# Kernel optimization log

Measured on AMD Instinct MI355X. Metric: run time of the kernel, lower is better.

The kernel has to match this reference:

```python
import jax, jax.numpy as jnp
import numpy as np

SR = 48000
SEG = 960
NH = 8
BASE = 440.0
F0_MIN = 20.0
F0_MAX = 16000.0
EPS = 1e-4
N, C, LF = 16, 256, 200


def _interp_linear(x, Lw):
    # Matches torch F.interpolate(mode='linear', align_corners=False).
    # x: (N, C, Lf) -> (N, C, Lw)
    Lf = x.shape[-1]
    scale = Lf / Lw
    src = (jnp.arange(Lw, dtype=x.dtype) + 0.5) * scale - 0.5
    src = jnp.clip(src, 0.0, Lf - 1)
    i0 = jnp.floor(src).astype(jnp.int32)
    i1 = jnp.minimum(i0 + 1, Lf - 1)
    w = src - i0.astype(x.dtype)
    return x[..., i0] * (1.0 - w) + x[..., i1] * w


def setup_inputs() -> dict:
    key = jax.random.key(0)
    ks = jax.random.split(key, 7)
    scale = 1.0 / np.sqrt(C)
    return {
        "x": jax.random.normal(ks[0], (N, C, LF), dtype=jnp.float32),
        "mag_w": jax.random.uniform(ks[1], (NH, C), jnp.float32, -scale, scale),
        "mag_b": jax.random.uniform(ks[2], (NH,), jnp.float32, -scale, scale),
        "cn_scale": jnp.ones((1, C, 1), jnp.float32),
        "cn_shift": jnp.zeros((1, C, 1), jnp.float32),
        "oct_w": jax.random.uniform(ks[3], (1, C), jnp.float32, -scale, scale),
        "oct_b": jax.random.uniform(ks[4], (1,), jnp.float32, -scale, scale),
    }


def reference(x, mag_w, mag_b, cn_scale, cn_shift, oct_w, oct_b):
    n, c, Lf = x.shape
    Lw = Lf * SEG
    # ChannelNorm (torch.std is unbiased -> ddof=1)
    mu = jnp.mean(x, axis=1, keepdims=True)
    sigma = jnp.std(x, axis=1, keepdims=True, ddof=1) + EPS
    xn = (x - mu) / sigma * cn_scale + cn_shift
    # 1x1 convs
    octave = jnp.einsum('ncl,oc->nol', xn, oct_w) + oct_b[None, :, None]  # (N,1,Lf)
    mag = jnp.exp(jnp.minimum(jnp.einsum('ncl,hc->nhl', x, mag_w) + mag_b[None, :, None], 6.0))  # (N,NH,Lf)
    f0 = jnp.clip(BASE * jnp.exp2(octave), F0_MIN, F0_MAX)  # (N,1,Lf)
    mul = jnp.arange(1, NH + 1, dtype=x.dtype)[None, :, None]
    formants = f0 * mul  # (N,NH,Lf)
    formants_w = _interp_linear(formants, Lw)  # (N,NH,Lw)
    mag_w_up = _interp_linear(mag, Lw)         # (N,NH,Lw)
    t = jnp.cumsum(formants_w / SR, axis=2)
    harmonics = jnp.sin(2.0 * jnp.pi * t) * mag_w_up
    wave = jnp.mean(harmonics, axis=1, keepdims=True)  # (N,1,Lw)
    return wave
```

## Files before the change

kernel.cpp:

```cpp
#include <hip/hip_runtime.h>
#include <math.h>


#define NB   16
#define CCH  256
#define LFR  200
#define LW   192000
#define NHH  8
#define NKM  201
#define INV_SR (1.0 / 48000.0)
#define PSTRIDE 20

__device__ inline double wave_sum64(double v) {
    #pragma unroll
    for (int off = 32; off > 0; off >>= 1) v += __shfl_xor(v, off);
    return v;
}
__device__ inline double wave_incl_scan64(double v) {
    int lane = threadIdx.x & 63;
    #pragma unroll
    for (int off = 1; off < 64; off <<= 1) {
        double t = __shfl_up(v, off);
        if (lane >= off) v += t;
    }
    return v;
}

__global__ __launch_bounds__(1024)
void hg_prep(const float* __restrict__ x,
             const float* __restrict__ mag_w, const float* __restrict__ mag_b,
             const float* __restrict__ cn_scale, const float* __restrict__ cn_shift,
             const float* __restrict__ oct_w, const float* __restrict__ oct_b,
             float* __restrict__ params) {
    __shared__ double w2l[CCH];
    __shared__ double psum[4][256], psumsq[4][256], pdotx[4][256];
    __shared__ float  pmag[NHH][4][256];
    __shared__ double redA[4], redB[4];
    __shared__ double SAB[2];
    __shared__ double Fl[LFR];
    __shared__ double Tl[LFR];
    __shared__ float  Mgl[LFR][NHH];

    int n   = blockIdx.x;
    int tid = threadIdx.x;
    int t   = tid & 255;
    int g   = tid >> 8;
    int lane = tid & 63;
    int wv  = tid >> 6;

    double sa = 0.0, sb = 0.0;
    if (tid < CCH) {
        double sc = (double)cn_scale[tid];
        double sh = (double)cn_shift[tid];
        double ow = (double)oct_w[tid];
        double w2 = sc * ow;
        w2l[tid] = w2;
        sa = w2;
        sb = sh * ow;
    }
    sa = wave_sum64(sa);
    sb = wave_sum64(sb);
    if (tid < CCH && lane == 0) { redA[wv] = sa; redB[wv] = sb; }
    __syncthreads();
    if (tid == 0) {
        SAB[0] = redA[0] + redA[1] + redA[2] + redA[3];
        SAB[1] = redB[0] + redB[1] + redB[2] + redB[3];
    }

    int gs = __builtin_amdgcn_readfirstlane(g);
    const float* xb = x + (size_t)n * CCH * LFR;
    double s = 0.0, s2 = 0.0, dx = 0.0;
    float zm[NHH] = {0.f, 0.f, 0.f, 0.f, 0.f, 0.f, 0.f, 0.f};
    #pragma unroll 4
    for (int cc = 0; cc < 64; cc++) {
        int c = gs * 64 + cc;
        float xf = (t < LFR) ? xb[c * LFR + t] : 0.f;
        double xd = (double)xf;
        s  += xd;
        s2  = fma(xd, xd, s2);
        dx  = fma(xd, w2l[c], dx);
        #pragma unroll
        for (int h = 0; h < NHH; h++)
            zm[h] = fmaf(xf, mag_w[h * CCH + c], zm[h]);
    }
    psum[g][t] = s; psumsq[g][t] = s2; pdotx[g][t] = dx;
    #pragma unroll
    for (int h = 0; h < NHH; h++) pmag[h][g][t] = zm[h];
    __syncthreads();

    if (tid < LFR) {
        double sum = psum[0][tid] + psum[1][tid] + psum[2][tid] + psum[3][tid];
        double ssq = psumsq[0][tid] + psumsq[1][tid] + psumsq[2][tid] + psumsq[3][tid];
        double dot = pdotx[0][tid] + pdotx[1][tid] + pdotx[2][tid] + pdotx[3][tid];
        double mu  = sum * (1.0 / 256.0);
        double var = (ssq - sum * mu) * (1.0 / 255.0);
        double inv = 1.0 / (sqrt(var) + 1e-4);
        double oct = inv * (dot - mu * SAB[0]) + SAB[1] + (double)oct_b[0];
        double f0  = 440.0 * exp2(oct);
        f0 = fmin(fmax(f0, 20.0), 16000.0);
        Fl[tid] = f0;
        #pragma unroll
        for (int h = 0; h < NHH; h++) {
            float z = pmag[h][0][tid] + pmag[h][1][tid] + pmag[h][2][tid]
                    + pmag[h][3][tid] + mag_b[h];
            Mgl[tid][h] = expf(fminf(z, 6.f));
        }
    }
    __syncthreads();

    if (tid < 64) {
        double carry = 480.0 * Fl[0];
        for (int base = 0; base < LFR; base += 64) {
            int k = base + tid;
            double d = (k < LFR - 1) ? 480.0 * (Fl[k] + Fl[k + 1]) : 0.0;
            double scn = wave_incl_scan64(d);
            if (k < LFR) Tl[k] = carry + scn - d;
            carry += __shfl(scn, 63);
        }
    }
    __syncthreads();

    if (tid < NKM) {
        int km = tid;
        int kc = min(max(km - 1, 0), LFR - 1);
        bool body = (km >= 1 && km <= LFR - 1);
        double Sd = Fl[kc] * INV_SR;
        double Qd = body ? (Fl[km] - Fl[km - 1]) * (INV_SR / 1920.0) : 0.0;
        double Pd = (km == 0) ? (-480.0 * Fl[0] * INV_SR) : Tl[km - 1] * INV_SR;
        double Pp = Pd + 480.0 * Sd + 230400.0 * Qd;
        double Sp = Sd + 960.0 * Qd;
        float* pr = params + ((size_t)n * NKM + km) * PSTRIDE;
        pr[0] = (float)(Pp - floor(Pp));
        pr[1] = (float)Sp;
        pr[2] = (float)Qd;
        pr[3] = 0.f;
        #pragma unroll
        for (int h = 0; h < NHH; h++) {
            float a = Mgl[kc][h];
            pr[4 + h]  = a;
            pr[12 + h] = body ? (Mgl[km][h] - a) : 0.f;
        }
    }
}

__global__ __launch_bounds__(256)
void hg_wave(const float* __restrict__ params, float* __restrict__ out) {
    int km = blockIdx.x, n = blockIdx.y;
    const float4* pb = (const float4*)(params + ((size_t)n * NKM + km) * PSTRIDE);
    float4 v0 = pb[0], v1 = pb[1], v2 = pb[2], v3 = pb[3], v4 = pb[4];
    float Pf = v0.x, Sf = v0.y, Qf = v0.z;
    float ma[NHH] = {v1.x, v1.y, v1.z, v1.w, v2.x, v2.y, v2.z, v2.w};
    float md[NHH] = {v3.x, v3.y, v3.z, v3.w, v4.x, v4.y, v4.z, v4.w};

    int jstart = 960 * km - 480; if (jstart < 0) jstart = 0;
    int jend   = 960 * km + 480; if (jend > LW)  jend = LW;
    int pcbase = 1 - 960 * km;
    float* outn = out + (size_t)n * LW;

    for (int j = jstart + (int)threadIdx.x; j < jend; j += 256) {
        float pc = (float)(j + pcbase);
        float t1 = fmaf(Qf, pc, Sf);
        float tb = fmaf(pc, t1, Pf);
        float fr;
        asm("v_fract_f32 %0, %1" : "=v"(fr) : "v"(tb));
        float w = (pc + 479.5f) * (1.0f / 960.0f);
        float acc = 0.f;
        #pragma unroll
        for (int h = 0; h < NHH; h++) {
            float fh = fr * (float)(h + 1);
            float sv;
            asm("v_fract_f32 %0, %1\n\tv_sin_f32 %0, %0" : "=v"(sv) : "v"(fh));
            acc = fmaf(fmaf(md[h], w, ma[h]), sv, acc);
        }
        outn[j] = acc * 0.125f;
    }
}

extern "C" void kernel_launch(void* const* d_in, const int* in_sizes, int n_in,
                              void* d_out, int out_size, void* d_ws, size_t ws_size,
                              hipStream_t stream) {
    const float* x        = (const float*)d_in[0];
    const float* mag_w    = (const float*)d_in[1];
    const float* mag_b    = (const float*)d_in[2];
    const float* cn_scale = (const float*)d_in[3];
    const float* cn_shift = (const float*)d_in[4];
    const float* oct_w    = (const float*)d_in[5];
    const float* oct_b    = (const float*)d_in[6];
    float* out = (float*)d_out;

    float* params = (float*)d_ws;

    hg_prep<<<dim3(NB), dim3(1024), 0, stream>>>(
        x, mag_w, mag_b, cn_scale, cn_shift, oct_w, oct_b, params);
    hg_wave<<<dim3(NKM, NB), dim3(256), 0, stream>>>(params, out);
}
```

Baseline: 27.37 us.

## Split channel reduction across more blocks and vectorize wave stores

```diff
diff --git a/kernel.cpp b/kernel.cpp
--- a/kernel.cpp
+++ b/kernel.cpp
@@ -8,6 +8,8 @@
 #define LW   192000
 #define NHH  8
 #define NKM  201
+#define CG   8
+#define CPB  32
 #define INV_SR (1.0 / 48000.0)
 #define PSTRIDE 20
 
@@ -26,84 +28,89 @@
     return v;
 }
 
-__global__ __launch_bounds__(1024)
-void hg_prep(const float* __restrict__ x,
-             const float* __restrict__ mag_w, const float* __restrict__ mag_b,
-             const float* __restrict__ cn_scale, const float* __restrict__ cn_shift,
-             const float* __restrict__ oct_w, const float* __restrict__ oct_b,
-             float* __restrict__ params) {
-    __shared__ double w2l[CCH];
-    __shared__ double psum[4][256], psumsq[4][256], pdotx[4][256];
-    __shared__ float  pmag[NHH][4][256];
-    __shared__ double redA[4], redB[4];
-    __shared__ double SAB[2];
+__global__ __launch_bounds__(256)
+void hg_partial(const float* __restrict__ x,
+                const float* __restrict__ mag_w,
+                const float* __restrict__ cn_scale,
+                const float* __restrict__ oct_w,
+                double* __restrict__ ps, double* __restrict__ ps2,
+                double* __restrict__ pdx, float* __restrict__ pmg) {
+    int n = blockIdx.x, cg = blockIdx.y;
+    int t = threadIdx.x;
+    const float* xb = x + (size_t)n * CCH * LFR;
+    int cbase = cg * CPB;
+
+    double s = 0.0, s2 = 0.0, dx = 0.0;
+    float zm[NHH] = {0.f, 0.f, 0.f, 0.f, 0.f, 0.f, 0.f, 0.f};
+    #pragma unroll 8
+    for (int cc = 0; cc < CPB; cc++) {
+        int c = cbase + cc;
+        float xf = (t < LFR) ? xb[(size_t)c * LFR + t] : 0.f;
+        double xd = (double)xf;
+        double w2 = (double)cn_scale[c] * (double)oct_w[c];
+        s += xd;
+        s2 = fma(xd, xd, s2);
+        dx = fma(xd, w2, dx);
+        #pragma unroll
+        for (int h = 0; h < NHH; h++)
+            zm[h] = fmaf(xf, mag_w[h * CCH + c], zm[h]);
+    }
+    size_t pi = ((size_t)n * CG + cg) * 256 + t;
+    ps[pi] = s; ps2[pi] = s2; pdx[pi] = dx;
+    #pragma unroll
+    for (int h = 0; h < NHH; h++)
+        pmg[(((size_t)n * CG + cg) * NHH + h) * 256 + t] = zm[h];
+}
+
+__global__ __launch_bounds__(256)
+void hg_tables(const double* __restrict__ ps, const double* __restrict__ ps2,
+               const double* __restrict__ pdx, const float* __restrict__ pmg,
+               const float* __restrict__ mag_b,
+               const float* __restrict__ cn_scale, const float* __restrict__ cn_shift,
+               const float* __restrict__ oct_w, const float* __restrict__ oct_b,
+               float* __restrict__ params) {
     __shared__ double Fl[LFR];
     __shared__ double Tl[LFR];
     __shared__ float  Mgl[LFR][NHH];
-
-    int n   = blockIdx.x;
-    int tid = threadIdx.x;
-    int t   = tid & 255;
-    int g   = tid >> 8;
-    int lane = tid & 63;
-    int wv  = tid >> 6;
-
-    double sa = 0.0, sb = 0.0;
-    if (tid < CCH) {
-        double sc = (double)cn_scale[tid];
-        double sh = (double)cn_shift[tid];
-        double ow = (double)oct_w[tid];
-        double w2 = sc * ow;
-        w2l[tid] = w2;
-        sa = w2;
-        sb = sh * ow;
-    }
-    sa = wave_sum64(sa);
-    sb = wave_sum64(sb);
-    if (tid < CCH && lane == 0) { redA[wv] = sa; redB[wv] = sb; }
+    __shared__ double SAB[2];
+
+    int n = blockIdx.x, tid = threadIdx.x;
+
+    if (tid < 64) {
+        double sa = 0.0, sb = 0.0;
+        #pragma unroll
+        for (int k = 0; k < 4; k++) {
+            int c = tid + 64 * k;
+            double ow = (double)oct_w[c];
+            sa = fma((double)cn_scale[c], ow, sa);
+            sb = fma((double)cn_shift[c], ow, sb);
+        }
+        sa = wave_sum64(sa);
+        sb = wave_sum64(sb);
+        if (tid == 0) { SAB[0] = sa; SAB[1] = sb; }
+    }
     __syncthreads();
-    if (tid == 0) {
-        SAB[0] = redA[0] + redA[1] + redA[2] + redA[3];
-        SAB[1] = redB[0] + redB[1] + redB[2] + redB[3];
-    }
-
-    int gs = __builtin_amdgcn_readfirstlane(g);
-    const float* xb = x + (size_t)n * CCH * LFR;
-    double s = 0.0, s2 = 0.0, dx = 0.0;
-    float zm[NHH] = {0.f, 0.f, 0.f, 0.f, 0.f, 0.f, 0.f, 0.f};
-    #pragma unroll 4
-    for (int cc = 0; cc < 64; cc++) {
-        int c = gs * 64 + cc;
-        float xf = (t < LFR) ? xb[c * LFR + t] : 0.f;
-        double xd = (double)xf;
-        s  += xd;
-        s2  = fma(xd, xd, s2);
-        dx  = fma(xd, w2l[c], dx);
-        #pragma unroll
-        for (int h = 0; h < NHH; h++)
-            zm[h] = fmaf(xf, mag_w[h * CCH + c], zm[h]);
-    }
-    psum[g][t] = s; psumsq[g][t] = s2; pdotx[g][t] = dx;
-    #pragma unroll
-    for (int h = 0; h < NHH; h++) pmag[h][g][t] = zm[h];
-    __syncthreads();
 
     if (tid < LFR) {
-        double sum = psum[0][tid] + psum[1][tid] + psum[2][tid] + psum[3][tid];
-        double ssq = psumsq[0][tid] + psumsq[1][tid] + psumsq[2][tid] + psumsq[3][tid];
-        double dot = pdotx[0][tid] + pdotx[1][tid] + pdotx[2][tid] + pdotx[3][tid];
-        double mu  = sum * (1.0 / 256.0);
-        double var = (ssq - sum * mu) * (1.0 / 255.0);
+        double s = 0.0, s2 = 0.0, dx = 0.0;
+        #pragma unroll
+        for (int cg = 0; cg < CG; cg++) {
+            size_t pi = ((size_t)n * CG + cg) * 256 + tid;
+            s += ps[pi]; s2 += ps2[pi]; dx += pdx[pi];
+        }
+        double mu  = s * (1.0 / 256.0);
+        double var = (s2 - s * mu) * (1.0 / 255.0);
         double inv = 1.0 / (sqrt(var) + 1e-4);
-        double oct = inv * (dot - mu * SAB[0]) + SAB[1] + (double)oct_b[0];
+        double oct = inv * (dx - mu * SAB[0]) + SAB[1] + (double)oct_b[0];
         double f0  = 440.0 * exp2(oct);
-        f0 = fmin(fmax(f0, 20.0), 16000.0);
-        Fl[tid] = f0;
+        Fl[tid] = fmin(fmax(f0, 20.0), 16000.0);
         #pragma unroll
         for (int h = 0; h < NHH; h++) {
-            float z = pmag[h][0][tid] + pmag[h][1][tid] + pmag[h][2][tid]
-                    + pmag[h][3][tid] + mag_b[h];
-            Mgl[tid][h] = expf(fminf(z, 6.f));
+            float z = 0.f;
+            #pragma unroll
+            for (int cg = 0; cg < CG; cg++)
+                z += pmg[(((size_t)n * CG + cg) * NHH + h) * 256 + tid];
+            Mgl[tid][h] = expf(fminf(z + mag_b[h], 6.f));
         }
     }
     __syncthreads();
@@ -152,15 +159,16 @@
     float ma[NHH] = {v1.x, v1.y, v1.z, v1.w, v2.x, v2.y, v2.z, v2.w};
     float md[NHH] = {v3.x, v3.y, v3.z, v3.w, v4.x, v4.y, v4.z, v4.w};
 
-    int jstart = 960 * km - 480; if (jstart < 0) jstart = 0;
-    int jend   = 960 * km + 480; if (jend > LW)  jend = LW;
-    int pcbase = 1 - 960 * km;
-    float* outn = out + (size_t)n * LW;
-
-    for (int j = jstart + (int)threadIdx.x; j < jend; j += 256) {
-        float pc = (float)(j + pcbase);
-        float t1 = fmaf(Qf, pc, Sf);
-        float tb = fmaf(pc, t1, Pf);
+    int tid = threadIdx.x;
+    if (tid >= 240) return;
+    int j0 = 960 * km - 480 + tid * 4;
+    if (j0 < 0 || j0 >= LW) return;
+
+    float r[4];
+    #pragma unroll
+    for (int u = 0; u < 4; u++) {
+        float pc = (float)(tid * 4 - 479 + u);
+        float tb = fmaf(pc, fmaf(Qf, pc, Sf), Pf);
         float fr;
         asm("v_fract_f32 %0, %1" : "=v"(fr) : "v"(tb));
         float w = (pc + 479.5f) * (1.0f / 960.0f);
@@ -172,8 +180,9 @@
             asm("v_fract_f32 %0, %1\n\tv_sin_f32 %0, %0" : "=v"(sv) : "v"(fh));
             acc = fmaf(fmaf(md[h], w, ma[h]), sv, acc);
         }
-        outn[j] = acc * 0.125f;
-    }
+        r[u] = acc * 0.125f;
+    }
+    *(float4*)(out + (size_t)n * LW + j0) = make_float4(r[0], r[1], r[2], r[3]);
 }
 
 extern "C" void kernel_launch(void* const* d_in, const int* in_sizes, int n_in,
@@ -188,9 +197,15 @@
     const float* oct_b    = (const float*)d_in[6];
     float* out = (float*)d_out;
 
-    float* params = (float*)d_ws;
-
-    hg_prep<<<dim3(NB), dim3(1024), 0, stream>>>(
-        x, mag_w, mag_b, cn_scale, cn_shift, oct_w, oct_b, params);
+    double* ps  = (double*)d_ws;
+    double* ps2 = ps  + (size_t)NB * CG * 256;
+    double* pdx = ps2 + (size_t)NB * CG * 256;
+    float*  pmg = (float*)(pdx + (size_t)NB * CG * 256);
+    float*  params = pmg + (size_t)NB * CG * NHH * 256;
+
+    hg_partial<<<dim3(NB, CG), dim3(256), 0, stream>>>(
+        x, mag_w, cn_scale, oct_w, ps, ps2, pdx, pmg);
+    hg_tables<<<dim3(NB), dim3(256), 0, stream>>>(
+        ps, ps2, pdx, pmg, mag_b, cn_scale, cn_shift, oct_w, oct_b, params);
     hg_wave<<<dim3(NKM, NB), dim3(256), 0, stream>>>(params, out);
 }
```

After: 23.06 us. -15.8%, faster.
